# Kernel tuning notes

Measured on AMD Instinct MI355X. Metric: run time of the kernel, lower is better.

## Reference

```python
import jax, jax.numpy as jnp
import numpy as np

N, E, IN, H, OUT, G = 40000, 640000, 128, 128, 16, 64


def _sage(x, src, dst, Wl, Wr, b, n):
    # PyG SAGEConv (aggr='mean'): out = lin_l(mean_j x_j) + lin_r(x_i); bias in lin_l only
    msg = jnp.take(x, src, axis=0)                      # [E, d] gather
    s = jax.ops.segment_sum(msg, dst, num_segments=n)   # [N, d] scatter-add
    cnt = jax.ops.segment_sum(jnp.ones((src.shape[0], 1), x.dtype), dst, num_segments=n)
    agg = s / jnp.maximum(cnt, 1.0)                     # mean; 0 for isolated nodes
    return agg @ Wl.T + x @ Wr.T + b


def setup_inputs() -> dict:
    key = jax.random.key(0)
    ks = jax.random.split(key, 12)
    x = jax.random.normal(ks[0], (N, IN), jnp.float32)
    edge_index = jax.random.randint(ks[1], (2, E), 0, N, jnp.int64)
    batch = jnp.sort(jax.random.randint(ks[2], (N,), 0, G, jnp.int64))
    def lin(k, o, i):
        return jax.random.normal(k, (o, i), jnp.float32) / np.sqrt(i)
    return {
        "x": x, "edge_index": edge_index, "batch": batch,
        "W1l": lin(ks[3], H, IN), "W1r": lin(ks[4], H, IN), "b1": jnp.zeros((H,), jnp.float32),
        "W2l": lin(ks[5], H, H),  "W2r": lin(ks[6], H, H),  "b2": jnp.zeros((H,), jnp.float32),
        "W3l": lin(ks[7], H, H),  "W3r": lin(ks[8], H, H),  "b3": jnp.zeros((H,), jnp.float32),
        "Wfc": lin(ks[9], OUT, H), "bfc": jnp.zeros((OUT,), jnp.float32),
    }


def reference(x, edge_index, batch, W1l, W1r, b1, W2l, W2r, b2, W3l, W3r, b3, Wfc, bfc):
    src, dst = edge_index[0], edge_index[1]
    n = x.shape[0]
    h = jax.nn.relu(_sage(x, src, dst, W1l, W1r, b1, n))
    h = jax.nn.relu(_sage(h, src, dst, W2l, W2r, b2, n))
    h = jax.nn.relu(_sage(h, src, dst, W3l, W3r, b3, n))
    # global_mean_pool over graph ids
    s = jax.ops.segment_sum(h, batch, num_segments=G)
    cnt = jax.ops.segment_sum(jnp.ones((n, 1), h.dtype), batch, num_segments=G)
    pooled = s / jnp.maximum(cnt, 1.0)                  # [G, H]
    return pooled @ Wfc.T + bfc                          # [G, OUT]
```

## Files before the change

### kernel.cpp

```cpp
#include <hip/hip_runtime.h>

static constexpr int D = 128;
static constexpr int PS = 32;

typedef __attribute__((ext_vector_type(8))) short short8;
typedef __attribute__((ext_vector_type(4))) float f32x4;

__device__ inline ushort f2bf(float f) {
  union { float f; unsigned u; } v; v.f = f;
  unsigned r = v.u + 0x7FFF + ((v.u >> 16) & 1);
  return (ushort)(r >> 16);
}
__device__ inline float bf2f_lo(unsigned p) {
  union { unsigned u; float f; } v; v.u = p << 16; return v.f;
}
__device__ inline float bf2f_hi(unsigned p) {
  union { unsigned u; float f; } v; v.u = p & 0xFFFF0000u; return v.f;
}

struct WPtrs { const float* s[6]; ushort* d[6]; };

__global__ __launch_bounds__(256) void k_prep(const float* __restrict__ x, ushort* __restrict__ xb, WPtrs p,
                                              const int* __restrict__ dst, int* __restrict__ hist,
                                              int n4x, int E) {
  int b = blockIdx.x, tid = threadIdx.x;
  int nxb = (n4x + 255) / 256;
  if (b < nxb) {
    int i = b * 256 + tid;
    if (i < n4x) {
      float4 v = *(const float4*)&x[i * 4];
      ushort4 o;
      o.x = f2bf(v.x); o.y = f2bf(v.y); o.z = f2bf(v.z); o.w = f2bf(v.w);
      *(ushort4*)&xb[i * 4] = o;
    }
  } else if (b < nxb + 96) {
    int idx = (b - nxb) * 256 + tid;
    int mat = idx >> 12;
    int off = (idx & 4095) * 4;
    float4 v = *(const float4*)&p.s[mat][off];
    ushort4 o;
    o.x = f2bf(v.x); o.y = f2bf(v.y); o.z = f2bf(v.z); o.w = f2bf(v.w);
    *(ushort4*)&p.d[mat][off] = o;
  } else {
    int e = (b - nxb - 96) * 256 + tid;
    if (e < E) atomicAdd(&hist[dst[e]], 1);
  }
}

__global__ __launch_bounds__(1024) void k_scan(const int* __restrict__ hist, int* __restrict__ offsets, int n) {
  __shared__ int wsum[16];
  int tid = threadIdx.x, lane = tid & 63, w = tid >> 6;
  int carry = 0;
  for (int base = 0; base < n; base += 8192) {
    int i0 = base + tid * 8;
    int v[8];
    #pragma unroll
    for (int j = 0; j < 8; ++j) { int i = i0 + j; v[j] = (i < n) ? hist[i] : 0; }
    int s = 0;
    #pragma unroll
    for (int j = 0; j < 8; ++j) { int t = v[j]; v[j] = s; s += t; }
    int x = s;
    #pragma unroll
    for (int off = 1; off < 64; off <<= 1) {
      int t = __shfl_up(x, off);
      if (lane >= off) x += t;
    }
    if (lane == 63) wsum[w] = x;
    __syncthreads();
    int wpre = 0, total = 0;
    #pragma unroll
    for (int k = 0; k < 16; ++k) { int t = wsum[k]; total += t; if (k < w) wpre += t; }
    int pre = carry + wpre + x - s;
    #pragma unroll
    for (int j = 0; j < 8; ++j) { int i = i0 + j; if (i < n) offsets[i] = pre + v[j]; }
    carry += total;
    __syncthreads();
  }
  if (tid == 0) offsets[n] = carry;
}

__global__ __launch_bounds__(256) void k_fill(const int* __restrict__ src, const int* __restrict__ dst,
                                              const int* __restrict__ offsets, int* __restrict__ cursor,
                                              int* __restrict__ ssrc, int E) {
  int e = blockIdx.x * 256 + threadIdx.x;
  if (e < E) {
    int d = dst[e];
    int pos = offsets[d] + atomicAdd(&cursor[d], 1);
    ssrc[pos] = src[e];
  }
}

__global__ __launch_bounds__(256) void k_aggregate_bf(const ushort* __restrict__ X, const int* __restrict__ offsets,
                                                      const int* __restrict__ ssrc, ushort* __restrict__ Agg, int n) {
  int wid = (blockIdx.x * 256 + threadIdx.x) >> 6;
  int lane = threadIdx.x & 63;
  if (wid >= n) return;
  int q = lane >> 4, r = lane & 15;
  int o0 = offsets[wid], deg = offsets[wid + 1] - o0;

  float acc[8];
  #pragma unroll
  for (int i = 0; i < 8; ++i) acc[i] = 0.f;

  for (int c0 = 0; c0 < deg; c0 += 64) {
    int cn = min(64, deg - c0);
    int myid = (lane < cn) ? ssrc[o0 + c0 + lane] : 0;
    for (int j = 0; j < cn; j += 16) {
      uint4 buf[4];
      #pragma unroll
      for (int t = 0; t < 4; ++t) {
        int e = j + t * 4 + q;
        buf[t] = (uint4){0u, 0u, 0u, 0u};
        if (e < cn) {
          int s = __shfl(myid, e);
          buf[t] = *(const uint4*)&X[(size_t)s * D + r * 8];
        }
      }
      #pragma unroll
      for (int t = 0; t < 4; ++t) {
        acc[0] += bf2f_lo(buf[t].x); acc[1] += bf2f_hi(buf[t].x);
        acc[2] += bf2f_lo(buf[t].y); acc[3] += bf2f_hi(buf[t].y);
        acc[4] += bf2f_lo(buf[t].z); acc[5] += bf2f_hi(buf[t].z);
        acc[6] += bf2f_lo(buf[t].w); acc[7] += bf2f_hi(buf[t].w);
      }
    }
  }
  #pragma unroll
  for (int i = 0; i < 8; ++i) {
    acc[i] += __shfl_xor(acc[i], 16);
    acc[i] += __shfl_xor(acc[i], 32);
  }
  if (q == 0) {
    float inv = 1.f / (float)max(deg, 1);
    uint4 o;
    o.x = (unsigned)f2bf(acc[0] * inv) | ((unsigned)f2bf(acc[1] * inv) << 16);
    o.y = (unsigned)f2bf(acc[2] * inv) | ((unsigned)f2bf(acc[3] * inv) << 16);
    o.z = (unsigned)f2bf(acc[4] * inv) | ((unsigned)f2bf(acc[5] * inv) << 16);
    o.w = (unsigned)f2bf(acc[6] * inv) | ((unsigned)f2bf(acc[7] * inv) << 16);
    *(uint4*)&Agg[(size_t)wid * D + r * 8] = o;
  }
}

__global__ __launch_bounds__(256) void k_gemm_mfma(const ushort* __restrict__ Abf, const ushort* __restrict__ Xbf,
                                                   const ushort* __restrict__ Wl, const ushort* __restrict__ Wr,
                                                   const float* __restrict__ bias, ushort* __restrict__ Out, int n) {
  int tid = threadIdx.x;
  int wave = tid >> 6, lane = tid & 63;
  int wm = wave >> 1, wn = wave & 1;
  int m_base = blockIdx.x * 64 + wm * 32;
  int n_base = wn * 64;
  int r = lane & 15, kg = lane >> 4;

  f32x4 acc[2][4];
  #pragma unroll
  for (int i = 0; i < 2; ++i)
    #pragma unroll
    for (int j = 0; j < 4; ++j) acc[i][j] = (f32x4){0.f, 0.f, 0.f, 0.f};

  const ushort* As[2] = {Abf, Xbf};
  const ushort* Ws[2] = {Wl, Wr};
  #pragma unroll
  for (int half = 0; half < 2; ++half) {
    const ushort* A = As[half];
    const ushort* W = Ws[half];
    #pragma unroll
    for (int k0 = 0; k0 < 128; k0 += 32) {
      int kk = k0 + kg * 8;
      short8 a[2], b[4];
      #pragma unroll
      for (int fm = 0; fm < 2; ++fm)
        a[fm] = *(const short8*)&A[(size_t)(m_base + fm * 16 + r) * D + kk];
      #pragma unroll
      for (int fn = 0; fn < 4; ++fn)
        b[fn] = *(const short8*)&W[(size_t)(n_base + fn * 16 + r) * D + kk];
      #pragma unroll
      for (int fm = 0; fm < 2; ++fm)
        #pragma unroll
        for (int fn = 0; fn < 4; ++fn)
          acc[fm][fn] = __builtin_amdgcn_mfma_f32_16x16x32_bf16(a[fm], b[fn], acc[fm][fn], 0, 0, 0);
    }
  }
  #pragma unroll
  for (int fn = 0; fn < 4; ++fn) {
    int j = n_base + fn * 16 + r;
    float bj = bias[j];
    #pragma unroll
    for (int fm = 0; fm < 2; ++fm) {
      #pragma unroll
      for (int q = 0; q < 4; ++q) {
        int node = m_base + fm * 16 + kg * 4 + q;
        float v = fmaxf(acc[fm][fn][q] + bj, 0.f);
        Out[(size_t)node * D + j] = f2bf(v);
      }
    }
  }
}

__global__ __launch_bounds__(256) void k_pool_partial(const ushort* __restrict__ H, const int* __restrict__ batch,
                                                      float* __restrict__ partial, int n) {
  __shared__ float wsums[4][128];
  int g = blockIdx.x / PS, s = blockIdx.x % PS;
  int tid = threadIdx.x, wave = tid >> 6, lane = tid & 63;
  int a = 0, b = n;
  while (a < b) { int m = (a + b) >> 1; if (batch[m] < g) a = m + 1; else b = m; }
  int lo = a;
  b = n;
  while (a < b) { int m = (a + b) >> 1; if (batch[m] < g + 1) a = m + 1; else b = m; }
  int hi = a;
  int len = hi - lo;
  int chunk = (len + PS - 1) / PS;
  int a0 = lo + s * chunk;
  int a1 = min(a0 + chunk, hi);
  float ax = 0.f, ay = 0.f;
  for (int node = a0 + wave; node < a1; node += 4) {
    unsigned v = *(const unsigned*)&H[(size_t)node * D + lane * 2];
    ax += bf2f_lo(v);
    ay += bf2f_hi(v);
  }
  wsums[wave][lane * 2] = ax;
  wsums[wave][lane * 2 + 1] = ay;
  __syncthreads();
  if (tid < 128) {
    float v = wsums[0][tid] + wsums[1][tid] + wsums[2][tid] + wsums[3][tid];
    partial[(size_t)blockIdx.x * 128 + tid] = v;
  }
}

__global__ __launch_bounds__(256) void k_pool_fc2(const float* __restrict__ partial, const int* __restrict__ batch,
                                                  const float* __restrict__ Wfc, const float* __restrict__ bfc,
                                                  float* __restrict__ out, int n, int OUT) {
  __shared__ float pooled[128];
  int g = blockIdx.x;
  int tid = threadIdx.x, lane = tid & 63;
  int a = 0, b = n;
  while (a < b) { int m = (a + b) >> 1; if (batch[m] < g) a = m + 1; else b = m; }
  int lo = a;
  b = n;
  while (a < b) { int m = (a + b) >> 1; if (batch[m] < g + 1) a = m + 1; else b = m; }
  int hi = a;
  float inv = 1.f / (float)max(hi - lo, 1);
  if (tid < 128) {
    float v = 0.f;
    #pragma unroll
    for (int s = 0; s < PS; ++s) v += partial[(size_t)(g * PS + s) * 128 + tid];
    pooled[tid] = v * inv;
  }
  __syncthreads();
  if (tid < 64) {
    float2 p = *(const float2*)&pooled[lane * 2];
    for (int o = 0; o < OUT; ++o) {
      float2 w = *(const float2*)&Wfc[o * D + lane * 2];
      float part = p.x * w.x + p.y * w.y;
      #pragma unroll
      for (int off = 32; off > 0; off >>= 1) part += __shfl_down(part, off);
      if (lane == 0) out[g * OUT + o] = part + bfc[o];
    }
  }
}

extern "C" void kernel_launch(void* const* d_in, const int* in_sizes, int n_in,
                              void* d_out, int out_size, void* d_ws, size_t ws_size,
                              hipStream_t stream) {
  const float* x   = (const float*)d_in[0];
  const int* ei    = (const int*)d_in[1];
  const int* batch = (const int*)d_in[2];
  const float* W1l = (const float*)d_in[3];
  const float* W1r = (const float*)d_in[4];
  const float* b1  = (const float*)d_in[5];
  const float* W2l = (const float*)d_in[6];
  const float* W2r = (const float*)d_in[7];
  const float* b2  = (const float*)d_in[8];
  const float* W3l = (const float*)d_in[9];
  const float* W3r = (const float*)d_in[10];
  const float* b3  = (const float*)d_in[11];
  const float* Wfc = (const float*)d_in[12];
  const float* bfc = (const float*)d_in[13];
  float* out = (float*)d_out;

  int N = in_sizes[0] / D;
  int E = in_sizes[1] / 2;
  int OUT = in_sizes[12] / D;
  int G = out_size / OUT;
  const int* src = ei;
  const int* dst = ei + E;

  ushort* xb  = (ushort*)d_ws;
  ushort* agg = xb + (size_t)N * D;
  ushort* h1  = agg + (size_t)N * D;
  ushort* h2  = h1 + (size_t)N * D;
  ushort* wb  = h2 + (size_t)N * D;
  int* ssrc   = (int*)(wb + 6 * 128 * 128);
  int* hist   = ssrc + E;
  int* cursor = hist + N;
  int* offsets = cursor + N;
  float* partial = (float*)(offsets + N + 2);

  ushort* wl1 = wb + 0 * 16384; ushort* wr1 = wb + 1 * 16384;
  ushort* wl2 = wb + 2 * 16384; ushort* wr2 = wb + 3 * 16384;
  ushort* wl3 = wb + 4 * 16384; ushort* wr3 = wb + 5 * 16384;

  hipMemsetAsync(hist, 0, (size_t)2 * N * 4, stream);

  WPtrs wp;
  wp.s[0] = W1l; wp.s[1] = W1r; wp.s[2] = W2l; wp.s[3] = W2r; wp.s[4] = W3l; wp.s[5] = W3r;
  wp.d[0] = wl1; wp.d[1] = wr1; wp.d[2] = wl2; wp.d[3] = wr2; wp.d[4] = wl3; wp.d[5] = wr3;

  int n4 = N * D / 4;
  int nxb = (n4 + 255) / 256;
  int eb = (E + 255) / 256;
  k_prep<<<nxb + 96 + eb, 256, 0, stream>>>(x, xb, wp, dst, hist, n4, E);
  k_scan<<<1, 1024, 0, stream>>>(hist, offsets, N);
  k_fill<<<eb, 256, 0, stream>>>(src, dst, offsets, cursor, ssrc, E);

  int ab = (N * 64 + 255) / 256;
  int gb = N / 64;

  k_aggregate_bf<<<ab, 256, 0, stream>>>(xb, offsets, ssrc, agg, N);
  k_gemm_mfma<<<gb, 256, 0, stream>>>(agg, xb, wl1, wr1, b1, h1, N);

  k_aggregate_bf<<<ab, 256, 0, stream>>>(h1, offsets, ssrc, agg, N);
  k_gemm_mfma<<<gb, 256, 0, stream>>>(agg, h1, wl2, wr2, b2, h2, N);

  k_aggregate_bf<<<ab, 256, 0, stream>>>(h2, offsets, ssrc, agg, N);
  k_gemm_mfma<<<gb, 256, 0, stream>>>(agg, h2, wl3, wr3, b3, h1, N);

  k_pool_partial<<<G * PS, 256, 0, stream>>>(h1, batch, partial, N);
  k_pool_fc2<<<G, 256, 0, stream>>>(partial, batch, Wfc, bfc, out, N, OUT);
}
```

Measured before the change: 263.1 us.

## Fuse mean aggregation and dual-linear MFMA GEMM into one per-layer kernel

Merges the gather-mean aggregation kernel and the MFMA GEMM kernel into one kernel per layer. Each block aggregates 64 nodes into a shared-memory bf16 tile and then runs the GEMM with A read from LDS, so the aggregated matrix never goes through global memory and three launches are removed. The cost is far fewer blocks for the gather phase: 625 blocks, each wave handling 16 nodes in sequence instead of one wave per node. That lowers latency hiding for the irregular gathers, and the barrier between phases stops them overlapping within a block.

After: 321.3 us. 22.1% more time.

```diff
diff --git a/kernel.cpp b/kernel.cpp
--- a/kernel.cpp
+++ b/kernel.cpp
@@ -90,66 +90,70 @@
   }
 }
 
-__global__ __launch_bounds__(256) void k_aggregate_bf(const ushort* __restrict__ X, const int* __restrict__ offsets,
-                                                      const int* __restrict__ ssrc, ushort* __restrict__ Agg, int n) {
-  int wid = (blockIdx.x * 256 + threadIdx.x) >> 6;
-  int lane = threadIdx.x & 63;
-  if (wid >= n) return;
+__global__ __launch_bounds__(256) void k_layer(const ushort* __restrict__ Xin,
+                                               const int* __restrict__ offsets, const int* __restrict__ ssrc,
+                                               const ushort* __restrict__ Wl, const ushort* __restrict__ Wr,
+                                               const float* __restrict__ bias, ushort* __restrict__ Out, int n) {
+  __shared__ ushort atile[64][136];
+  int tid = threadIdx.x;
+  int wave = tid >> 6, lane = tid & 63;
   int q = lane >> 4, r = lane & 15;
-  int o0 = offsets[wid], deg = offsets[wid + 1] - o0;
-
-  float acc[8];
-  #pragma unroll
-  for (int i = 0; i < 8; ++i) acc[i] = 0.f;
-
-  for (int c0 = 0; c0 < deg; c0 += 64) {
-    int cn = min(64, deg - c0);
-    int myid = (lane < cn) ? ssrc[o0 + c0 + lane] : 0;
-    for (int j = 0; j < cn; j += 16) {
-      uint4 buf[4];
-      #pragma unroll
-      for (int t = 0; t < 4; ++t) {
-        int e = j + t * 4 + q;
-        buf[t] = (uint4){0u, 0u, 0u, 0u};
-        if (e < cn) {
-          int s = __shfl(myid, e);
-          buf[t] = *(const uint4*)&X[(size_t)s * D + r * 8];
+  int base = blockIdx.x * 64;
+
+  for (int i = 0; i < 16; ++i) {
+    int node = base + wave * 16 + i;
+    float acc[8];
+    #pragma unroll
+    for (int t = 0; t < 8; ++t) acc[t] = 0.f;
+    int deg = 0;
+    if (node < n) {
+      int o0 = offsets[node];
+      deg = offsets[node + 1] - o0;
+      for (int c0 = 0; c0 < deg; c0 += 64) {
+        int cn = min(64, deg - c0);
+        int myid = (lane < cn) ? ssrc[o0 + c0 + lane] : 0;
+        for (int j = 0; j < cn; j += 16) {
+          uint4 buf[4];
+          #pragma unroll
+          for (int t = 0; t < 4; ++t) {
+            int e = j + t * 4 + q;
+            buf[t] = (uint4){0u, 0u, 0u, 0u};
+            if (e < cn) {
+              int s = __shfl(myid, e);
+              buf[t] = *(const uint4*)&Xin[(size_t)s * D + r * 8];
+            }
+          }
+          #pragma unroll
+          for (int t = 0; t < 4; ++t) {
+            acc[0] += bf2f_lo(buf[t].x); acc[1] += bf2f_hi(buf[t].x);
+            acc[2] += bf2f_lo(buf[t].y); acc[3] += bf2f_hi(buf[t].y);
+            acc[4] += bf2f_lo(buf[t].z); acc[5] += bf2f_hi(buf[t].z);
+            acc[6] += bf2f_lo(buf[t].w); acc[7] += bf2f_hi(buf[t].w);
+          }
         }
       }
-      #pragma unroll
-      for (int t = 0; t < 4; ++t) {
-        acc[0] += bf2f_lo(buf[t].x); acc[1] += bf2f_hi(buf[t].x);
-        acc[2] += bf2f_lo(buf[t].y); acc[3] += bf2f_hi(buf[t].y);
-        acc[4] += bf2f_lo(buf[t].z); acc[5] += bf2f_hi(buf[t].z);
-        acc[6] += bf2f_lo(buf[t].w); acc[7] += bf2f_hi(buf[t].w);
-      }
-    }
-  }
-  #pragma unroll
-  for (int i = 0; i < 8; ++i) {
-    acc[i] += __shfl_xor(acc[i], 16);
-    acc[i] += __shfl_xor(acc[i], 32);
-  }
-  if (q == 0) {
-    float inv = 1.f / (float)max(deg, 1);
-    uint4 o;
-    o.x = (unsigned)f2bf(acc[0] * inv) | ((unsigned)f2bf(acc[1] * inv) << 16);
-    o.y = (unsigned)f2bf(acc[2] * inv) | ((unsigned)f2bf(acc[3] * inv) << 16);
-    o.z = (unsigned)f2bf(acc[4] * inv) | ((unsigned)f2bf(acc[5] * inv) << 16);
-    o.w = (unsigned)f2bf(acc[6] * inv) | ((unsigned)f2bf(acc[7] * inv) << 16);
-    *(uint4*)&Agg[(size_t)wid * D + r * 8] = o;
-  }
-}
-
-__global__ __launch_bounds__(256) void k_gemm_mfma(const ushort* __restrict__ Abf, const ushort* __restrict__ Xbf,
-                                                   const ushort* __restrict__ Wl, const ushort* __restrict__ Wr,
-                                                   const float* __restrict__ bias, ushort* __restrict__ Out, int n) {
-  int tid = threadIdx.x;
-  int wave = tid >> 6, lane = tid & 63;
+    }
+    #pragma unroll
+    for (int t = 0; t < 8; ++t) {
+      acc[t] += __shfl_xor(acc[t], 16);
+      acc[t] += __shfl_xor(acc[t], 32);
+    }
+    if (q == 0) {
+      float inv = 1.f / (float)max(deg, 1);
+      uint4 o;
+      o.x = (unsigned)f2bf(acc[0] * inv) | ((unsigned)f2bf(acc[1] * inv) << 16);
+      o.y = (unsigned)f2bf(acc[2] * inv) | ((unsigned)f2bf(acc[3] * inv) << 16);
+      o.z = (unsigned)f2bf(acc[4] * inv) | ((unsigned)f2bf(acc[5] * inv) << 16);
+      o.w = (unsigned)f2bf(acc[6] * inv) | ((unsigned)f2bf(acc[7] * inv) << 16);
+      *(uint4*)&atile[wave * 16 + i][r * 8] = o;
+    }
+  }
+  __syncthreads();
+
   int wm = wave >> 1, wn = wave & 1;
-  int m_base = blockIdx.x * 64 + wm * 32;
+  int m_base = base + wm * 32;
   int n_base = wn * 64;
-  int r = lane & 15, kg = lane >> 4;
+  int kg = lane >> 4;
 
   f32x4 acc[2][4];
   #pragma unroll
@@ -157,28 +161,27 @@
     #pragma unroll
     for (int j = 0; j < 4; ++j) acc[i][j] = (f32x4){0.f, 0.f, 0.f, 0.f};
 
-  const ushort* As[2] = {Abf, Xbf};
-  const ushort* Ws[2] = {Wl, Wr};
   #pragma unroll
-  for (int half = 0; half < 2; ++half) {
-    const ushort* A = As[half];
-    const ushort* W = Ws[half];
-    #pragma unroll
-    for (int k0 = 0; k0 < 128; k0 += 32) {
-      int kk = k0 + kg * 8;
-      short8 a[2], b[4];
+  for (int k0 = 0; k0 < 128; k0 += 32) {
+    int kk = k0 + kg * 8;
+    short8 a0[2], a1[2], b0[4], b1[4];
+    #pragma unroll
+    for (int fm = 0; fm < 2; ++fm) {
+      a0[fm] = *(const short8*)&atile[wm * 32 + fm * 16 + r][kk];
+      a1[fm] = *(const short8*)&Xin[(size_t)(m_base + fm * 16 + r) * D + kk];
+    }
+    #pragma unroll
+    for (int fn = 0; fn < 4; ++fn) {
+      b0[fn] = *(const short8*)&Wl[(size_t)(n_base + fn * 16 + r) * D + kk];
+      b1[fn] = *(const short8*)&Wr[(size_t)(n_base + fn * 16 + r) * D + kk];
+    }
+    #pragma unroll
+    for (int fm = 0; fm < 2; ++fm)
       #pragma unroll
-      for (int fm = 0; fm < 2; ++fm)
-        a[fm] = *(const short8*)&A[(size_t)(m_base + fm * 16 + r) * D + kk];
-      #pragma unroll
-      for (int fn = 0; fn < 4; ++fn)
-        b[fn] = *(const short8*)&W[(size_t)(n_base + fn * 16 + r) * D + kk];
-      #pragma unroll
-      for (int fm = 0; fm < 2; ++fm)
-        #pragma unroll
-        for (int fn = 0; fn < 4; ++fn)
-          acc[fm][fn] = __builtin_amdgcn_mfma_f32_16x16x32_bf16(a[fm], b[fn], acc[fm][fn], 0, 0, 0);
-    }
+      for (int fn = 0; fn < 4; ++fn) {
+        acc[fm][fn] = __builtin_amdgcn_mfma_f32_16x16x32_bf16(a0[fm], b0[fn], acc[fm][fn], 0, 0, 0);
+        acc[fm][fn] = __builtin_amdgcn_mfma_f32_16x16x32_bf16(a1[fm], b1[fn], acc[fm][fn], 0, 0, 0);
+      }
   }
   #pragma unroll
   for (int fn = 0; fn < 4; ++fn) {
@@ -187,10 +190,12 @@
     #pragma unroll
     for (int fm = 0; fm < 2; ++fm) {
       #pragma unroll
-      for (int q = 0; q < 4; ++q) {
-        int node = m_base + fm * 16 + kg * 4 + q;
-        float v = fmaxf(acc[fm][fn][q] + bj, 0.f);
-        Out[(size_t)node * D + j] = f2bf(v);
+      for (int p = 0; p < 4; ++p) {
+        int node = m_base + fm * 16 + kg * 4 + p;
+        if (node < n) {
+          float v = fmaxf(acc[fm][fn][p] + bj, 0.f);
+          Out[(size_t)node * D + j] = f2bf(v);
+        }
       }
     }
   }
@@ -285,8 +290,7 @@
   const int* dst = ei + E;
 
   ushort* xb  = (ushort*)d_ws;
-  ushort* agg = xb + (size_t)N * D;
-  ushort* h1  = agg + (size_t)N * D;
+  ushort* h1  = xb + (size_t)N * D;
   ushort* h2  = h1 + (size_t)N * D;
   ushort* wb  = h2 + (size_t)N * D;
   int* ssrc   = (int*)(wb + 6 * 128 * 128);
@@ -312,17 +316,10 @@
   k_scan<<<1, 1024, 0, stream>>>(hist, offsets, N);
   k_fill<<<eb, 256, 0, stream>>>(src, dst, offsets, cursor, ssrc, E);
 
-  int ab = (N * 64 + 255) / 256;
-  int gb = N / 64;
-
-  k_aggregate_bf<<<ab, 256, 0, stream>>>(xb, offsets, ssrc, agg, N);
-  k_gemm_mfma<<<gb, 256, 0, stream>>>(agg, xb, wl1, wr1, b1, h1, N);
-
-  k_aggregate_bf<<<ab, 256, 0, stream>>>(h1, offsets, ssrc, agg, N);
-  k_gemm_mfma<<<gb, 256, 0, stream>>>(agg, h1, wl2, wr2, b2, h2, N);
-
-  k_aggregate_bf<<<ab, 256, 0, stream>>>(h2, offsets, ssrc, agg, N);
-  k_gemm_mfma<<<gb, 256, 0, stream>>>(agg, h2, wl3, wr3, b3, h1, N);
+  int gb = (N + 63) / 64;
+  k_layer<<<gb, 256, 0, stream>>>(xb, offsets, ssrc, wl1, wr1, b1, h1, N);
+  k_layer<<<gb, 256, 0, stream>>>(h1, offsets, ssrc, wl2, wr2, b2, h2, N);
+  k_layer<<<gb, 256, 0, stream>>>(h2, offsets, ssrc, wl3, wr3, b3, h1, N);
 
   k_pool_partial<<<G * PS, 256, 0, stream>>>(h1, batch, partial, N);
   k_pool_fc2<<<G, 256, 0, stream>>>(partial, batch, Wfc, bfc, out, N, OUT);
```

## Aggregate two nodes per wave and split GEMM output columns across blocks

Applied to the files above, without the earlier changes.

The aggregation kernel now has each wavefront process two destination nodes, interleaving their neighbor gathers so more independent loads are in flight and wave-level overhead is amortized. The cost is load imbalance from iterating to the larger degree, plus doubled accumulator registers. Separately, the MFMA GEMM halves the per-wave N tile and launches twice as many blocks, each covering half the output columns. This raises parallelism and occupancy but re-reads the A rows once per column half.

Result: slower. 294.0 us (+11.8%).

```diff
diff --git a/kernel.cpp b/kernel.cpp
--- a/kernel.cpp
+++ b/kernel.cpp
@@ -92,52 +92,83 @@
 
 __global__ __launch_bounds__(256) void k_aggregate_bf(const ushort* __restrict__ X, const int* __restrict__ offsets,
                                                       const int* __restrict__ ssrc, ushort* __restrict__ Agg, int n) {
-  int wid = (blockIdx.x * 256 + threadIdx.x) >> 6;
+  int wpair = (blockIdx.x * 256 + threadIdx.x) >> 6;
   int lane = threadIdx.x & 63;
-  if (wid >= n) return;
+  int nA = wpair * 2, nB = nA + 1;
+  if (nA >= n) return;
   int q = lane >> 4, r = lane & 15;
-  int o0 = offsets[wid], deg = offsets[wid + 1] - o0;
-
-  float acc[8];
-  #pragma unroll
-  for (int i = 0; i < 8; ++i) acc[i] = 0.f;
-
-  for (int c0 = 0; c0 < deg; c0 += 64) {
-    int cn = min(64, deg - c0);
-    int myid = (lane < cn) ? ssrc[o0 + c0 + lane] : 0;
-    for (int j = 0; j < cn; j += 16) {
-      uint4 buf[4];
+
+  int oA0 = offsets[nA], degA = offsets[nA + 1] - oA0;
+  int oB0 = 0, degB = 0;
+  if (nB < n) { oB0 = offsets[nB]; degB = offsets[nB + 1] - oB0; }
+
+  float accA[8], accB[8];
+  #pragma unroll
+  for (int i = 0; i < 8; ++i) { accA[i] = 0.f; accB[i] = 0.f; }
+
+  int dmax = max(degA, degB);
+  for (int c0 = 0; c0 < dmax; c0 += 64) {
+    int cnA = min(64, degA - c0);
+    int cnB = min(64, degB - c0);
+    int idA = (lane < cnA) ? ssrc[oA0 + c0 + lane] : 0;
+    int idB = (lane < cnB) ? ssrc[oB0 + c0 + lane] : 0;
+    int cmax = max(cnA, cnB);
+    for (int j = 0; j < cmax; j += 16) {
+      uint4 bufA[4], bufB[4];
       #pragma unroll
       for (int t = 0; t < 4; ++t) {
         int e = j + t * 4 + q;
-        buf[t] = (uint4){0u, 0u, 0u, 0u};
-        if (e < cn) {
-          int s = __shfl(myid, e);
-          buf[t] = *(const uint4*)&X[(size_t)s * D + r * 8];
+        bufA[t] = (uint4){0u, 0u, 0u, 0u};
+        if (e < cnA) {
+          int s = __shfl(idA, e);
+          bufA[t] = *(const uint4*)&X[(size_t)s * D + r * 8];
         }
       }
       #pragma unroll
       for (int t = 0; t < 4; ++t) {
-        acc[0] += bf2f_lo(buf[t].x); acc[1] += bf2f_hi(buf[t].x);
-        acc[2] += bf2f_lo(buf[t].y); acc[3] += bf2f_hi(buf[t].y);
-        acc[4] += bf2f_lo(buf[t].z); acc[5] += bf2f_hi(buf[t].z);
-        acc[6] += bf2f_lo(buf[t].w); acc[7] += bf2f_hi(buf[t].w);
+        int e = j + t * 4 + q;
+        bufB[t] = (uint4){0u, 0u, 0u, 0u};
+        if (e < cnB) {
+          int s = __shfl(idB, e);
+          bufB[t] = *(const uint4*)&X[(size_t)s * D + r * 8];
+        }
       }
+      #pragma unroll
+      for (int t = 0; t < 4; ++t) {
+        accA[0] += bf2f_lo(bufA[t].x); accA[1] += bf2f_hi(bufA[t].x);
+        accA[2] += bf2f_lo(bufA[t].y); accA[3] += bf2f_hi(bufA[t].y);
+        accA[4] += bf2f_lo(bufA[t].z); accA[5] += bf2f_hi(bufA[t].z);
+        accA[6] += bf2f_lo(bufA[t].w); accA[7] += bf2f_hi(bufA[t].w);
+        accB[0] += bf2f_lo(bufB[t].x); accB[1] += bf2f_hi(bufB[t].x);
+        accB[2] += bf2f_lo(bufB[t].y); accB[3] += bf2f_hi(bufB[t].y);
+        accB[4] += bf2f_lo(bufB[t].z); accB[5] += bf2f_hi(bufB[t].z);
+        accB[6] += bf2f_lo(bufB[t].w); accB[7] += bf2f_hi(bufB[t].w);
+      }
     }
   }
   #pragma unroll
   for (int i = 0; i < 8; ++i) {
-    acc[i] += __shfl_xor(acc[i], 16);
-    acc[i] += __shfl_xor(acc[i], 32);
+    accA[i] += __shfl_xor(accA[i], 16);
+    accA[i] += __shfl_xor(accA[i], 32);
+    accB[i] += __shfl_xor(accB[i], 16);
+    accB[i] += __shfl_xor(accB[i], 32);
   }
   if (q == 0) {
-    float inv = 1.f / (float)max(deg, 1);
+    float inv = 1.f / (float)max(degA, 1);
     uint4 o;
-    o.x = (unsigned)f2bf(acc[0] * inv) | ((unsigned)f2bf(acc[1] * inv) << 16);
-    o.y = (unsigned)f2bf(acc[2] * inv) | ((unsigned)f2bf(acc[3] * inv) << 16);
-    o.z = (unsigned)f2bf(acc[4] * inv) | ((unsigned)f2bf(acc[5] * inv) << 16);
-    o.w = (unsigned)f2bf(acc[6] * inv) | ((unsigned)f2bf(acc[7] * inv) << 16);
-    *(uint4*)&Agg[(size_t)wid * D + r * 8] = o;
+    o.x = (unsigned)f2bf(accA[0] * inv) | ((unsigned)f2bf(accA[1] * inv) << 16);
+    o.y = (unsigned)f2bf(accA[2] * inv) | ((unsigned)f2bf(accA[3] * inv) << 16);
+    o.z = (unsigned)f2bf(accA[4] * inv) | ((unsigned)f2bf(accA[5] * inv) << 16);
+    o.w = (unsigned)f2bf(accA[6] * inv) | ((unsigned)f2bf(accA[7] * inv) << 16);
+    *(uint4*)&Agg[(size_t)nA * D + r * 8] = o;
+  } else if (q == 1 && nB < n) {
+    float inv = 1.f / (float)max(degB, 1);
+    uint4 o;
+    o.x = (unsigned)f2bf(accB[0] * inv) | ((unsigned)f2bf(accB[1] * inv) << 16);
+    o.y = (unsigned)f2bf(accB[2] * inv) | ((unsigned)f2bf(accB[3] * inv) << 16);
+    o.z = (unsigned)f2bf(accB[4] * inv) | ((unsigned)f2bf(accB[5] * inv) << 16);
+    o.w = (unsigned)f2bf(accB[6] * inv) | ((unsigned)f2bf(accB[7] * inv) << 16);
+    *(uint4*)&Agg[(size_t)nB * D + r * 8] = o;
   }
 }
 
@@ -146,16 +177,17 @@
                                                    const float* __restrict__ bias, ushort* __restrict__ Out, int n) {
   int tid = threadIdx.x;
   int wave = tid >> 6, lane = tid & 63;
+  int mb = blockIdx.x >> 1, nh = blockIdx.x & 1;
   int wm = wave >> 1, wn = wave & 1;
-  int m_base = blockIdx.x * 64 + wm * 32;
-  int n_base = wn * 64;
+  int m_base = mb * 64 + wm * 32;
+  int n_base = nh * 64 + wn * 32;
   int r = lane & 15, kg = lane >> 4;
 
-  f32x4 acc[2][4];
+  f32x4 acc[2][2];
   #pragma unroll
   for (int i = 0; i < 2; ++i)
     #pragma unroll
-    for (int j = 0; j < 4; ++j) acc[i][j] = (f32x4){0.f, 0.f, 0.f, 0.f};
+    for (int j = 0; j < 2; ++j) acc[i][j] = (f32x4){0.f, 0.f, 0.f, 0.f};
 
   const ushort* As[2] = {Abf, Xbf};
   const ushort* Ws[2] = {Wl, Wr};
@@ -166,30 +198,30 @@
     #pragma unroll
     for (int k0 = 0; k0 < 128; k0 += 32) {
       int kk = k0 + kg * 8;
-      short8 a[2], b[4];
+      short8 a[2], b[2];
       #pragma unroll
       for (int fm = 0; fm < 2; ++fm)
         a[fm] = *(const short8*)&A[(size_t)(m_base + fm * 16 + r) * D + kk];
       #pragma unroll
-      for (int fn = 0; fn < 4; ++fn)
+      for (int fn = 0; fn < 2; ++fn)
         b[fn] = *(const short8*)&W[(size_t)(n_base + fn * 16 + r) * D + kk];
       #pragma unroll
       for (int fm = 0; fm < 2; ++fm)
         #pragma unroll
-        for (int fn = 0; fn < 4; ++fn)
+        for (int fn = 0; fn < 2; ++fn)
           acc[fm][fn] = __builtin_amdgcn_mfma_f32_16x16x32_bf16(a[fm], b[fn], acc[fm][fn], 0, 0, 0);
     }
   }
   #pragma unroll
-  for (int fn = 0; fn < 4; ++fn) {
+  for (int fn = 0; fn < 2; ++fn) {
     int j = n_base + fn * 16 + r;
     float bj = bias[j];
     #pragma unroll
     for (int fm = 0; fm < 2; ++fm) {
       #pragma unroll
-      for (int q = 0; q < 4; ++q) {
-        int node = m_base + fm * 16 + kg * 4 + q;
-        float v = fmaxf(acc[fm][fn][q] + bj, 0.f);
+      for (int p = 0; p < 4; ++p) {
+        int node = m_base + fm * 16 + kg * 4 + p;
+        float v = fmaxf(acc[fm][fn][p] + bj, 0.f);
         Out[(size_t)node * D + j] = f2bf(v);
       }
     }
@@ -312,8 +344,8 @@
   k_scan<<<1, 1024, 0, stream>>>(hist, offsets, N);
   k_fill<<<eb, 256, 0, stream>>>(src, dst, offsets, cursor, ssrc, E);
 
-  int ab = (N * 64 + 255) / 256;
-  int gb = N / 64;
+  int ab = (((N + 1) / 2) * 64 + 255) / 256;
+  int gb = ((N + 63) / 64) * 2;
 
   k_aggregate_bf<<<ab, 256, 0, stream>>>(xb, offsets, ssrc, agg, N);
   k_gemm_mfma<<<gb, 256, 0, stream>>>(agg, xb, wl1, wr1, b1, h1, N);
```
